# Kernel optimization log

Hardware: AMD Instinct MI355X
Metric: run time of the kernel (lower is better)

The kernel has to match this reference:

```python
import jax, jax.numpy as jnp
import numpy as np
import math

B, S, D = 4, 4096, 2048
H = 16
DH = D // H  # 128
EPS = 1e-5


def _layer_norm(x, g, b):
    m = jnp.mean(x, axis=-1, keepdims=True)
    v = jnp.mean(jnp.square(x - m), axis=-1, keepdims=True)
    return (x - m) * jax.lax.rsqrt(v + EPS) * g + b


def setup_inputs() -> dict:
    key = jax.random.key(0)
    ks = jax.random.split(key, 12)
    s = 0.02
    return {
        "X": jax.random.normal(ks[0], (B, S, D), dtype=jnp.float32),
        "Wq": jax.random.normal(ks[1], (D, D), dtype=jnp.float32) * s,
        "bq": jnp.zeros((D,), dtype=jnp.float32),
        "Wk": jax.random.normal(ks[2], (D, D), dtype=jnp.float32) * s,
        "bk": jnp.zeros((D,), dtype=jnp.float32),
        "Wv": jax.random.normal(ks[3], (D, D), dtype=jnp.float32) * s,
        "bv": jnp.zeros((D,), dtype=jnp.float32),
        "g1": jnp.ones((D,), dtype=jnp.float32),
        "beta1": jnp.zeros((D,), dtype=jnp.float32),
        "W1": jax.random.normal(ks[4], (D, D), dtype=jnp.float32) * s,
        "b1": jnp.zeros((D,), dtype=jnp.float32),
        "W2": jax.random.normal(ks[5], (D, D), dtype=jnp.float32) * s,
        "b2": jnp.zeros((D,), dtype=jnp.float32),
        "g2": jnp.ones((D,), dtype=jnp.float32),
        "beta2": jnp.zeros((D,), dtype=jnp.float32),
    }


def reference(X, Wq, bq, Wk, bk, Wv, bv, g1, beta1, W1, b1, W2, b2, g2, beta2):
    # --- MultiHeadSelfAttention (faithful: .view, so attention is over HEADS per token) ---
    q = (X @ Wq + bq).reshape(B, S, H, DH)
    k = (X @ Wk + bk).reshape(B, S, H, DH)
    v = (X @ Wv + bv).reshape(B, S, H, DH)
    # [B, S, H, H] scores: heads attend to heads within the same position
    att = jnp.einsum('bshd,bstd->bsht', q, k) / math.sqrt(DH)
    att = jax.nn.softmax(att, axis=-1)
    y = jnp.einsum('bsht,bstd->bshd', att, v).reshape(B, S, D)
    # --- residual + LN1 ---
    X1 = _layer_norm(X + y, g1, beta1)
    # --- FeedForward: D -> D -> D with exact GELU ---
    h = jax.nn.gelu(X1 @ W1 + b1, approximate=False)
    y2 = h @ W2 + b2
    # --- residual + LN2 ---
    return _layer_norm(X1 + y2, g2, beta2)
```

## Files before the change

kernel.cpp:

```cpp
#include <hip/hip_runtime.h>
#include <math.h>

#define DM 2048
#define NT 16384
#define KD 2048

typedef __bf16 bf16x8 __attribute__((ext_vector_type(8)));
typedef float  f32x4  __attribute__((ext_vector_type(4)));

__device__ __forceinline__ void gld_lds16(const void* g, void* l) {
  __builtin_amdgcn_global_load_lds(
      (const __attribute__((address_space(1))) unsigned int*)g,
      (__attribute__((address_space(3))) unsigned int*)l, 16, 0, 0);
}

__global__ __launch_bounds__(256) void k_cast(const float* __restrict__ x,
                                              __bf16* __restrict__ y) {
  const size_t i = ((size_t)blockIdx.x * 256 + threadIdx.x) * 8;
  const float4 a = *(const float4*)(x + i);
  const float4 b = *(const float4*)(x + i + 4);
  bf16x8 o;
  o[0]=(__bf16)a.x; o[1]=(__bf16)a.y; o[2]=(__bf16)a.z; o[3]=(__bf16)a.w;
  o[4]=(__bf16)b.x; o[5]=(__bf16)b.y; o[6]=(__bf16)b.z; o[7]=(__bf16)b.w;
  *(bf16x8*)(y + i) = o;
}

__global__ __launch_bounds__(256) void k_transpose(const float* __restrict__ W,
                                                   __bf16* __restrict__ Wt) {
  __shared__ float t[32][33];
  const int tx = threadIdx.x, ty = threadIdx.y;
  const int n  = blockIdx.x * 32 + tx;
  const int k0 = blockIdx.y * 32;
  #pragma unroll
  for (int j = 0; j < 32; j += 8) t[ty + j][tx] = W[(size_t)(k0 + ty + j) * DM + n];
  __syncthreads();
  const int kk = k0 + tx;
  const int n0 = blockIdx.x * 32;
  #pragma unroll
  for (int j = 0; j < 32; j += 8)
    Wt[(size_t)(n0 + ty + j) * KD + kk] = (__bf16)t[tx][ty + j];
}

__global__ __launch_bounds__(256) void k_bias3(const float* __restrict__ a,
                                               const float* __restrict__ b,
                                               const float* __restrict__ c,
                                               float* __restrict__ o) {
  const int i = blockIdx.x * 256 + threadIdx.x;
  o[i] = (i < 2048) ? a[i] : ((i < 4096) ? b[i - 2048] : c[i - 4096]);
}

__global__ __launch_bounds__(256, 2) void k_gemm(
    const __bf16* __restrict__ A, const __bf16* __restrict__ Bt,
    const float* __restrict__ bias, const int mode, const int ntile_n,
    const int NS,
    __bf16* __restrict__ outb, const float* __restrict__ resf,
    const __bf16* __restrict__ resb, float* __restrict__ outf) {
  __shared__ __bf16 As[128 * 32];
  __shared__ __bf16 Bs[128 * 32];
  const int tid  = threadIdx.x;
  const int wave = tid >> 6, lane = tid & 63;
  const int quad = lane >> 4, r16 = lane & 15;
  const int bid = blockIdx.x;
  const int m0 = (bid / ntile_n) * 128;
  const int n0 = (bid % ntile_n) * 128;
  const int wm = (wave >> 1) * 64, wn = (wave & 1) * 64;

  const int srow = tid >> 2;
  const int scol = (tid & 3) * 8;
  const __bf16* Ap0 = A  + (size_t)(m0 + srow) * KD + scol;
  const __bf16* Ap1 = A  + (size_t)(m0 + 64 + srow) * KD + scol;
  const __bf16* Bp0 = Bt + (size_t)(n0 + srow) * KD + scol;
  const __bf16* Bp1 = Bt + (size_t)(n0 + 64 + srow) * KD + scol;
  __bf16* AsW0 = &As[wave * 512];
  __bf16* AsW1 = &As[2048 + wave * 512];
  __bf16* BsW0 = &Bs[wave * 512];
  __bf16* BsW1 = &Bs[2048 + wave * 512];

  f32x4 acc[4][4] = {};

  for (int k0 = 0; k0 < KD; k0 += 32) {
    gld_lds16(Ap0 + k0, AsW0);
    gld_lds16(Ap1 + k0, AsW1);
    gld_lds16(Bp0 + k0, BsW0);
    gld_lds16(Bp1 + k0, BsW1);
    __syncthreads();
    bf16x8 af[4], bfr[4];
    #pragma unroll
    for (int mi = 0; mi < 4; mi++)
      af[mi] = *(const bf16x8*)&As[(wm + mi * 16 + r16) * 32 + quad * 8];
    #pragma unroll
    for (int ni = 0; ni < 4; ni++)
      bfr[ni] = *(const bf16x8*)&Bs[(wn + ni * 16 + r16) * 32 + quad * 8];
    #pragma unroll
    for (int mi = 0; mi < 4; mi++)
      #pragma unroll
      for (int ni = 0; ni < 4; ni++)
        acc[mi][ni] = __builtin_amdgcn_mfma_f32_16x16x32_bf16(af[mi], bfr[ni], acc[mi][ni], 0, 0, 0);
    __syncthreads();
  }

  if (mode <= 1) {
    __bf16* eb = (wave < 2) ? &As[wave * 2048] : &Bs[(wave - 2) * 2048];
    #pragma unroll
    for (int half = 0; half < 2; half++) {
      #pragma unroll
      for (int nj = 0; nj < 2; nj++) {
        const int ni = half * 2 + nj;
        const int gn = n0 + wn + ni * 16 + r16;
        const float bv = bias[gn];
        #pragma unroll
        for (int mi = 0; mi < 4; mi++) {
          #pragma unroll
          for (int r = 0; r < 4; r++) {
            float v = acc[mi][ni][r] + bv;
            if (mode == 1) v = 0.5f * v * (1.0f + erff(v * 0.70710678118654752f));
            eb[(mi * 16 + quad * 4 + r) * 32 + nj * 16 + r16] = (__bf16)v;
          }
        }
      }
      #pragma unroll
      for (int rd = 0; rd < 4; rd++) {
        const int row = rd * 16 + (lane >> 2);
        const int c0 = (lane & 3) * 8;
        bf16x8 vv = *(const bf16x8*)&eb[row * 32 + c0];
        *(bf16x8*)(outb + (size_t)(m0 + wm + row) * NS + n0 + wn + half * 32 + c0) = vv;
      }
    }
  } else {
    #pragma unroll
    for (int ni = 0; ni < 4; ni++) {
      const int gn = n0 + wn + ni * 16 + r16;
      const float bv = bias[gn];
      #pragma unroll
      for (int mi = 0; mi < 4; mi++) {
        const int gm = m0 + wm + mi * 16 + quad * 4;
        if (mode == 2) {
          #pragma unroll
          for (int r = 0; r < 4; r++) {
            const size_t o = (size_t)(gm + r) * NS + gn;
            outf[o] = acc[mi][ni][r] + bv + resf[o];
          }
        } else {
          #pragma unroll
          for (int r = 0; r < 4; r++) {
            const size_t o = (size_t)(gm + r) * NS + gn;
            outf[o] = acc[mi][ni][r] + bv + (float)resb[o];
          }
        }
      }
    }
  }
}

__global__ __launch_bounds__(256) void k_attn_ln1(
    const __bf16* __restrict__ QKV, const float* __restrict__ X,
    const float* __restrict__ g1, const float* __restrict__ be1,
    float* __restrict__ X1, __bf16* __restrict__ X1b, const int use_f32) {
  __shared__ float qs[16 * 132];
  __shared__ float ks[16 * 132];
  __shared__ float vs[16 * 132];
  __shared__ float p[256];
  __shared__ float red[8];
  const int tid = threadIdx.x;
  const size_t qbase = (size_t)blockIdx.x * 6144;
  const size_t base  = (size_t)blockIdx.x * DM;
  const int e0 = tid * 8;

  {
    const int row = e0 >> 7, c0 = e0 & 127;
    bf16x8 qv = *(const bf16x8*)(QKV + qbase + e0);
    bf16x8 kv = *(const bf16x8*)(QKV + qbase + 2048 + e0);
    bf16x8 vv = *(const bf16x8*)(QKV + qbase + 4096 + e0);
    #pragma unroll
    for (int j = 0; j < 8; j++) {
      qs[row * 132 + c0 + j] = (float)qv[j];
      ks[row * 132 + c0 + j] = (float)kv[j];
      vs[row * 132 + c0 + j] = (float)vv[j];
    }
  }
  __syncthreads();

  {
    const int h = tid >> 4, t = tid & 15;
    const float* qp = &qs[h * 132];
    const float* kp = &ks[t * 132];
    float s = 0.f;
    #pragma unroll
    for (int d = 0; d < 128; d++) s += qp[d] * kp[d];
    s *= 0.08838834764831845f;
    float mx = s;
    #pragma unroll
    for (int off = 8; off; off >>= 1) mx = fmaxf(mx, __shfl_xor(mx, off, 16));
    const float e = expf(s - mx);
    float sum = e;
    #pragma unroll
    for (int off = 8; off; off >>= 1) sum += __shfl_xor(sum, off, 16);
    p[tid] = e / sum;
  }
  __syncthreads();

  float zloc[8];
  float zs = 0.f, zq = 0.f;
  {
    const float4 x1 = *(const float4*)(X + base + e0);
    const float4 x2 = *(const float4*)(X + base + e0 + 4);
    const float xr[8] = {x1.x, x1.y, x1.z, x1.w, x2.x, x2.y, x2.z, x2.w};
    const int hh = e0 >> 7;
    const int d0 = e0 & 127;
    const float* pp = &p[hh * 16];
    #pragma unroll
    for (int j = 0; j < 8; j++) {
      float y = 0.f;
      #pragma unroll
      for (int t2 = 0; t2 < 16; t2++) y += pp[t2] * vs[t2 * 132 + d0 + j];
      const float z = xr[j] + y;
      zloc[j] = z; zs += z; zq += z * z;
    }
  }
  #pragma unroll
  for (int off = 32; off; off >>= 1) {
    zs += __shfl_xor(zs, off, 64);
    zq += __shfl_xor(zq, off, 64);
  }
  const int wave = tid >> 6, lane = tid & 63;
  if (lane == 0) { red[wave] = zs; red[4 + wave] = zq; }
  __syncthreads();
  zs = red[0] + red[1] + red[2] + red[3];
  zq = red[4] + red[5] + red[6] + red[7];
  const float mean = zs * (1.f / DM);
  const float var = zq * (1.f / DM) - mean * mean;
  const float rstd = rsqrtf(var + 1e-5f);
  {
    float o[8];
    #pragma unroll
    for (int j = 0; j < 8; j++)
      o[j] = (zloc[j] - mean) * rstd * g1[e0 + j] + be1[e0 + j];
    if (use_f32) {
      *(float4*)(X1 + base + e0)     = make_float4(o[0], o[1], o[2], o[3]);
      *(float4*)(X1 + base + e0 + 4) = make_float4(o[4], o[5], o[6], o[7]);
    }
    bf16x8 ob;
    #pragma unroll
    for (int j = 0; j < 8; j++) ob[j] = (__bf16)o[j];
    *(bf16x8*)(X1b + base + e0) = ob;
  }
}

__global__ __launch_bounds__(256) void k_ln2(const float* __restrict__ Z,
                                             const float* __restrict__ g,
                                             const float* __restrict__ be,
                                             float* __restrict__ out) {
  __shared__ float red[8];
  const int tid = threadIdx.x;
  const size_t base = (size_t)blockIdx.x * DM;
  const int e0 = tid * 8;
  const float4 a = *(const float4*)(Z + base + e0);
  const float4 b = *(const float4*)(Z + base + e0 + 4);
  float z[8] = {a.x, a.y, a.z, a.w, b.x, b.y, b.z, b.w};
  float zs = 0.f, zq = 0.f;
  #pragma unroll
  for (int j = 0; j < 8; j++) { zs += z[j]; zq += z[j] * z[j]; }
  #pragma unroll
  for (int off = 32; off; off >>= 1) {
    zs += __shfl_xor(zs, off, 64);
    zq += __shfl_xor(zq, off, 64);
  }
  const int wave = tid >> 6, lane = tid & 63;
  if (lane == 0) { red[wave] = zs; red[4 + wave] = zq; }
  __syncthreads();
  zs = red[0] + red[1] + red[2] + red[3];
  zq = red[4] + red[5] + red[6] + red[7];
  const float mean = zs * (1.f / DM);
  const float var = zq * (1.f / DM) - mean * mean;
  const float rstd = rsqrtf(var + 1e-5f);
  float o[8];
  #pragma unroll
  for (int j = 0; j < 8; j++)
    o[j] = (z[j] - mean) * rstd * g[e0 + j] + be[e0 + j];
  *(float4*)(out + base + e0)     = make_float4(o[0], o[1], o[2], o[3]);
  *(float4*)(out + base + e0 + 4) = make_float4(o[4], o[5], o[6], o[7]);
}

extern "C" void kernel_launch(void* const* d_in, const int* in_sizes, int n_in,
                              void* d_out, int out_size, void* d_ws, size_t ws_size,
                              hipStream_t stream) {
  const float* X   = (const float*)d_in[0];
  const float* Wq  = (const float*)d_in[1];
  const float* bq  = (const float*)d_in[2];
  const float* Wk  = (const float*)d_in[3];
  const float* bk  = (const float*)d_in[4];
  const float* Wv  = (const float*)d_in[5];
  const float* bv  = (const float*)d_in[6];
  const float* g1  = (const float*)d_in[7];
  const float* be1 = (const float*)d_in[8];
  const float* W1  = (const float*)d_in[9];
  const float* b1  = (const float*)d_in[10];
  const float* W2  = (const float*)d_in[11];
  const float* b2  = (const float*)d_in[12];
  const float* g2  = (const float*)d_in[13];
  const float* be2 = (const float*)d_in[14];
  float* out = (float*)d_out;

  char* ws = (char*)d_ws;
  size_t off = 0;
  auto alloc = [&](size_t b) -> char* {
    char* p = ws + off;
    off += (b + 255) & ~(size_t)255;
    return p;
  };
  const size_t EL  = (size_t)NT * DM;
  const size_t EL3 = (size_t)NT * 6144;
  __bf16* Xb    = (__bf16*)alloc(EL * 2);
  __bf16* Wqkvt = (__bf16*)alloc((size_t)6144 * KD * 2);
  __bf16* W1t   = (__bf16*)alloc((size_t)DM * KD * 2);
  __bf16* W2t   = (__bf16*)alloc((size_t)DM * KD * 2);
  float*  b3    = (float*)alloc(6144 * 4);
  __bf16* QKVb  = (__bf16*)alloc(EL3 * 2);
  __bf16* X1b   = (__bf16*)alloc(EL * 2);
  const int use_f32 = (ws_size >= off + EL * 4) ? 1 : 0;
  float* X1 = nullptr;
  if (use_f32) X1 = (float*)alloc(EL * 4);
  __bf16* Hb = Xb;
  float*  Z  = (float*)QKVb;

  k_cast<<<dim3(NT * DM / 2048), dim3(256), 0, stream>>>(X, Xb);
  dim3 tb(32, 8), tg(64, 64);
  k_transpose<<<tg, tb, 0, stream>>>(Wq, Wqkvt);
  k_transpose<<<tg, tb, 0, stream>>>(Wk, Wqkvt + (size_t)2048 * KD);
  k_transpose<<<tg, tb, 0, stream>>>(Wv, Wqkvt + (size_t)4096 * KD);
  k_transpose<<<tg, tb, 0, stream>>>(W1, W1t);
  k_transpose<<<tg, tb, 0, stream>>>(W2, W2t);
  k_bias3<<<dim3(24), dim3(256), 0, stream>>>(bq, bk, bv, b3);

  k_gemm<<<dim3((NT / 128) * 48), dim3(256), 0, stream>>>(
      Xb, Wqkvt, b3, 0, 48, 6144, QKVb, nullptr, nullptr, nullptr);
  k_attn_ln1<<<dim3(NT), dim3(256), 0, stream>>>(QKVb, X, g1, be1, X1, X1b, use_f32);
  k_gemm<<<dim3((NT / 128) * 16), dim3(256), 0, stream>>>(
      X1b, W1t, b1, 1, 16, 2048, Hb, nullptr, nullptr, nullptr);
  k_gemm<<<dim3((NT / 128) * 16), dim3(256), 0, stream>>>(
      Hb, W2t, b2, use_f32 ? 2 : 3, 16, 2048, nullptr, X1, X1b, Z);
  k_ln2<<<dim3(NT), dim3(256), 0, stream>>>(Z, g2, be2, out);
}
```

Before: 1.382 ms.

## Double GEMM K-tile to 64 with XOR-swizzled LDS layout

Each k-iteration of the bf16 MFMA GEMM now stages a 64-wide K slice instead of 32, which halves the number of barrier pairs per tile. Global-to-LDS loads place 16-byte chunks at XOR-swizzled positions, and fragment reads use the matching swizzle to avoid LDS bank conflicts on the 128-byte rows. The epilogue scratch buffer now fits entirely in As. LDS use doubles to 32 KB per block, which may limit occupancy, and there is still no double buffering.

New measurement: 1.231 ms. 1.12x faster.

```diff
diff --git a/kernel.cpp b/kernel.cpp
--- a/kernel.cpp
+++ b/kernel.cpp
@@ -55,8 +55,8 @@
     const int NS,
     __bf16* __restrict__ outb, const float* __restrict__ resf,
     const __bf16* __restrict__ resb, float* __restrict__ outf) {
-  __shared__ __bf16 As[128 * 32];
-  __shared__ __bf16 Bs[128 * 32];
+  __shared__ __bf16 As[128 * 64];
+  __shared__ __bf16 Bs[128 * 64];
   const int tid  = threadIdx.x;
   const int wave = tid >> 6, lane = tid & 63;
   const int quad = lane >> 4, r16 = lane & 15;
@@ -65,42 +65,51 @@
   const int n0 = (bid % ntile_n) * 128;
   const int wm = (wave >> 1) * 64, wn = (wave & 1) * 64;
 
-  const int srow = tid >> 2;
-  const int scol = (tid & 3) * 8;
-  const __bf16* Ap0 = A  + (size_t)(m0 + srow) * KD + scol;
-  const __bf16* Ap1 = A  + (size_t)(m0 + 64 + srow) * KD + scol;
-  const __bf16* Bp0 = Bt + (size_t)(n0 + srow) * KD + scol;
-  const __bf16* Bp1 = Bt + (size_t)(n0 + 64 + srow) * KD + scol;
-  __bf16* AsW0 = &As[wave * 512];
-  __bf16* AsW1 = &As[2048 + wave * 512];
-  __bf16* BsW0 = &Bs[wave * 512];
-  __bf16* BsW1 = &Bs[2048 + wave * 512];
+  const int lrow = lane >> 3;
+  const int gblk = (lane & 7) ^ lrow;
+  const __bf16* Ap[4];
+  const __bf16* Bp[4];
+  __bf16* AsW[4];
+  __bf16* BsW[4];
+  #pragma unroll
+  for (int i = 0; i < 4; i++) {
+    const int sr = i * 32 + wave * 8 + lrow;
+    Ap[i] = A  + (size_t)(m0 + sr) * KD + gblk * 8;
+    Bp[i] = Bt + (size_t)(n0 + sr) * KD + gblk * 8;
+    AsW[i] = &As[i * 2048 + wave * 512];
+    BsW[i] = &Bs[i * 2048 + wave * 512];
+  }
 
   f32x4 acc[4][4] = {};
 
-  for (int k0 = 0; k0 < KD; k0 += 32) {
-    gld_lds16(Ap0 + k0, AsW0);
-    gld_lds16(Ap1 + k0, AsW1);
-    gld_lds16(Bp0 + k0, BsW0);
-    gld_lds16(Bp1 + k0, BsW1);
+  for (int k0 = 0; k0 < KD; k0 += 64) {
+    #pragma unroll
+    for (int i = 0; i < 4; i++) {
+      gld_lds16(Ap[i] + k0, AsW[i]);
+      gld_lds16(Bp[i] + k0, BsW[i]);
+    }
     __syncthreads();
-    bf16x8 af[4], bfr[4];
-    #pragma unroll
-    for (int mi = 0; mi < 4; mi++)
-      af[mi] = *(const bf16x8*)&As[(wm + mi * 16 + r16) * 32 + quad * 8];
-    #pragma unroll
-    for (int ni = 0; ni < 4; ni++)
-      bfr[ni] = *(const bf16x8*)&Bs[(wn + ni * 16 + r16) * 32 + quad * 8];
-    #pragma unroll
-    for (int mi = 0; mi < 4; mi++)
+    #pragma unroll
+    for (int ks = 0; ks < 2; ks++) {
+      const int fb = ((ks * 4 + quad) ^ (r16 & 7)) * 8;
+      bf16x8 af[4], bfr[4];
+      #pragma unroll
+      for (int mi = 0; mi < 4; mi++)
+        af[mi] = *(const bf16x8*)&As[(wm + mi * 16 + r16) * 64 + fb];
       #pragma unroll
       for (int ni = 0; ni < 4; ni++)
-        acc[mi][ni] = __builtin_amdgcn_mfma_f32_16x16x32_bf16(af[mi], bfr[ni], acc[mi][ni], 0, 0, 0);
+        bfr[ni] = *(const bf16x8*)&Bs[(wn + ni * 16 + r16) * 64 + fb];
+      #pragma unroll
+      for (int mi = 0; mi < 4; mi++)
+        #pragma unroll
+        for (int ni = 0; ni < 4; ni++)
+          acc[mi][ni] = __builtin_amdgcn_mfma_f32_16x16x32_bf16(af[mi], bfr[ni], acc[mi][ni], 0, 0, 0);
+    }
     __syncthreads();
   }
 
   if (mode <= 1) {
-    __bf16* eb = (wave < 2) ? &As[wave * 2048] : &Bs[(wave - 2) * 2048];
+    __bf16* eb = &As[wave * 2048];
     #pragma unroll
     for (int half = 0; half < 2; half++) {
       #pragma unroll
```
